# Optimization experiments

Hardware: AMD Instinct MI355X
Metric: run time of the kernel (lower is better)

## Reference

```python
import jax, jax.numpy as jnp
import numpy as np

NEG = -1e6  # SequenceMask fill value from original code


def setup_inputs() -> dict:
    key = jax.random.key(0)
    ks = jax.random.split(key, 7)
    B, Tq, Tk, U = 32, 1024, 1024, 256
    return {
        "query": jax.random.normal(ks[0], (B, Tq, U), dtype=jnp.float32),
        "key": jax.random.normal(ks[1], (B, Tk, U), dtype=jnp.float32),
        "value": jax.random.normal(ks[2], (B, Tk, U), dtype=jnp.float32),
        "valid_length": jax.random.randint(ks[3], (B,), 0, Tk, dtype=jnp.int32),
        "W_k": jax.random.normal(ks[4], (U, U), dtype=jnp.float32) * (1.0 / np.sqrt(U)),
        "W_q": jax.random.normal(ks[5], (U, U), dtype=jnp.float32) * (1.0 / np.sqrt(U)),
        "v": jax.random.normal(ks[6], (U,), dtype=jnp.float32) * (1.0 / np.sqrt(U)),
    }


def reference(query, key, value, valid_length, W_k, W_q, v):
    # Original applies W_k to query and W_q to key (naming swap kept faithfully).
    tq = jnp.tanh(jnp.einsum('bqu,vu->bqv', query, W_k))  # (B,Tq,U)
    tk = jnp.tanh(jnp.einsum('bku,vu->bkv', key, W_q))    # (B,Tk,U)
    # v is linear over (tq_i + tk_j): decompose to avoid (B,Tq,Tk,U) tensor.
    sq = jnp.einsum('bqu,u->bq', tq, v)  # (B,Tq)
    sk = jnp.einsum('bku,u->bk', tk, v)  # (B,Tk)
    scores = sq[:, :, None] + sk[:, None, :]  # (B,Tq,Tk)
    Tk_ = key.shape[1]
    mask = jnp.arange(Tk_)[None, None, :] < valid_length[:, None, None]  # (B,1,Tk)
    scores = jnp.where(mask, scores, NEG)
    attn = jax.nn.softmax(scores, axis=-1)  # dropout p=0 (eval) -> identity
    return jnp.einsum('bqk,bkd->bqd', attn, value)
```

## Files before the change

kernel.cpp:

```cpp
#include <hip/hip_runtime.h>
#include <hip/hip_fp16.h>
#include <math.h>

#define NB 32
#define TQ 1024
#define TK 1024
#define UD 256

typedef __attribute__((ext_vector_type(8))) _Float16 f16x8;
typedef __attribute__((ext_vector_type(4))) float f32x4;

__device__ __forceinline__ float fast_tanh(float x) {
  const float e = __expf(2.0f * x);
  return 1.0f - 2.0f / (e + 1.0f);
}

__global__ __launch_bounds__(256, 2) void sk_mfma_kernel(
    const float* __restrict__ key, const float* __restrict__ Wq,
    const float* __restrict__ v, float* __restrict__ sk) {
  __shared__ _Float16 Bt[32768];

  const int tid = threadIdx.x;
  const int lane = tid & 63;
  const int wc = tid >> 6;
  const int lx = lane & 15;
  const int lg = lane >> 4;
  const int arow = blockIdx.x * 64 + wc * 16 + lx;
  const float* gA = key + (size_t)arow * UD + lg * 8;

  f32x4 acc[16];
#pragma unroll
  for (int n = 0; n < 16; ++n) acc[n] = (f32x4){0.f, 0.f, 0.f, 0.f};

  for (int p = 0; p < 2; ++p) {
    {
      const float* wrow = Wq + (size_t)tid * UD + p * 128;
#pragma unroll
      for (int it = 0; it < 16; ++it) {
        const float4 w0 = *reinterpret_cast<const float4*>(wrow + it * 8);
        const float4 w1 = *reinterpret_cast<const float4*>(wrow + it * 8 + 4);
        f16x8 h;
        h[0] = (_Float16)w0.x; h[1] = (_Float16)w0.y;
        h[2] = (_Float16)w0.z; h[3] = (_Float16)w0.w;
        h[4] = (_Float16)w1.x; h[5] = (_Float16)w1.y;
        h[6] = (_Float16)w1.z; h[7] = (_Float16)w1.w;
        *reinterpret_cast<f16x8*>(Bt + ((size_t)it * 256 + tid) * 8) = h;
      }
    }
    __syncthreads();

#pragma unroll
    for (int kc = 0; kc < 4; ++kc) {
      const int k0 = p * 128 + kc * 32;
      const float4 a0 = *reinterpret_cast<const float4*>(gA + k0);
      const float4 a1 = *reinterpret_cast<const float4*>(gA + k0 + 4);
      f16x8 af;
      af[0] = (_Float16)a0.x; af[1] = (_Float16)a0.y;
      af[2] = (_Float16)a0.z; af[3] = (_Float16)a0.w;
      af[4] = (_Float16)a1.x; af[5] = (_Float16)a1.y;
      af[6] = (_Float16)a1.z; af[7] = (_Float16)a1.w;
#pragma unroll
      for (int n = 0; n < 16; ++n) {
        const f16x8 bf = *reinterpret_cast<const f16x8*>(
            Bt + (((kc * 4 + lg) * 256) + n * 16 + lx) * 8);
        acc[n] =
            __builtin_amdgcn_mfma_f32_16x16x32_f16(af, bf, acc[n], 0, 0, 0);
      }
    }
    __syncthreads();
  }

  float out_r[4] = {0.f, 0.f, 0.f, 0.f};
#pragma unroll
  for (int n = 0; n < 16; ++n) {
    const float vn = v[n * 16 + lx];
#pragma unroll
    for (int r = 0; r < 4; ++r) out_r[r] += vn * fast_tanh(acc[n][r]);
  }
#pragma unroll
  for (int r = 0; r < 4; ++r) {
    float s = out_r[r];
    s += __shfl_xor(s, 1);
    s += __shfl_xor(s, 2);
    s += __shfl_xor(s, 4);
    s += __shfl_xor(s, 8);
    if (lx == 0) sk[blockIdx.x * 64 + wc * 16 + lg * 4 + r] = s;
  }
}

__global__ __launch_bounds__(256) void pv_bcast_kernel(
    const float* __restrict__ sk, const int* __restrict__ vlen,
    const float* __restrict__ value, float* __restrict__ out) {
  const int b = blockIdx.x >> 3;
  const int dc = blockIdx.x & 7;
  const int tid = threadIdx.x;
  const int vl = vlen[b];
  __shared__ float wbuf[1024];
  __shared__ float red4[8];
  __shared__ float racc[32][32];
  __shared__ float fin[32];
  const float* skb = sk + b * TK;

  if (vl == 0) {
#pragma unroll
    for (int idx = 0; idx < 4; ++idx) wbuf[tid + idx * 256] = 1.0f / (float)TK;
  } else {
    float m = -1e30f;
#pragma unroll
    for (int idx = 0; idx < 4; ++idx) {
      const int k = tid + idx * 256;
      if (k < vl) m = fmaxf(m, skb[k]);
    }
    for (int off = 1; off < 64; off <<= 1) m = fmaxf(m, __shfl_xor(m, off));
    if ((tid & 63) == 0) red4[tid >> 6] = m;
    __syncthreads();
    m = fmaxf(fmaxf(red4[0], red4[1]), fmaxf(red4[2], red4[3]));
    float e[4];
    float zs = 0.f;
#pragma unroll
    for (int idx = 0; idx < 4; ++idx) {
      const int k = tid + idx * 256;
      e[idx] = (k < vl) ? __expf(skb[k] - m) : 0.f;
      zs += e[idx];
    }
    for (int off = 1; off < 64; off <<= 1) zs += __shfl_xor(zs, off);
    if ((tid & 63) == 0) red4[4 + (tid >> 6)] = zs;
    __syncthreads();
    const float rz = 1.0f / (red4[4] + red4[5] + red4[6] + red4[7]);
#pragma unroll
    for (int idx = 0; idx < 4; ++idx) wbuf[tid + idx * 256] = e[idx] * rz;
  }
  __syncthreads();

  const int c = tid & 7;
  const int kg = tid >> 3;
  const float* vb = value + (size_t)b * TK * UD + dc * 32 + c * 4;
  float4 a = make_float4(0.f, 0.f, 0.f, 0.f);
#pragma unroll 8
  for (int i = 0; i < 32; ++i) {
    const int k = i * 32 + kg;
    const float wk = wbuf[k];
    const float4 x = *reinterpret_cast<const float4*>(vb + (size_t)k * UD);
    a.x = fmaf(wk, x.x, a.x);
    a.y = fmaf(wk, x.y, a.y);
    a.z = fmaf(wk, x.z, a.z);
    a.w = fmaf(wk, x.w, a.w);
  }
  racc[kg][c * 4 + 0] = a.x;
  racc[kg][c * 4 + 1] = a.y;
  racc[kg][c * 4 + 2] = a.z;
  racc[kg][c * 4 + 3] = a.w;
  __syncthreads();
  if (tid < 32) {
    float s = 0.f;
#pragma unroll
    for (int g = 0; g < 32; ++g) s += racc[g][tid];
    fin[tid] = s;
  }
  __syncthreads();

  const float4 f4 = *reinterpret_cast<const float4*>(&fin[c * 4]);
  float* ob = out + (size_t)b * TQ * UD + dc * 32 + c * 4;
#pragma unroll 8
  for (int i = 0; i < 32; ++i) {
    const int q = i * 32 + kg;
    *reinterpret_cast<float4*>(ob + (size_t)q * UD) = f4;
  }
}

extern "C" void kernel_launch(void* const* d_in, const int* in_sizes, int n_in,
                              void* d_out, int out_size, void* d_ws,
                              size_t ws_size, hipStream_t stream) {
  const float* key = (const float*)d_in[1];
  const float* value = (const float*)d_in[2];
  const int* vlen = (const int*)d_in[3];
  const float* Wq = (const float*)d_in[5];
  const float* v = (const float*)d_in[6];
  float* out = (float*)d_out;

  float* sk = (float*)d_ws;

  sk_mfma_kernel<<<(NB * TK) / 64, 256, 0, stream>>>(key, Wq, v, sk);
  pv_bcast_kernel<<<NB * 8, 256, 0, stream>>>(sk, vlen, value, out);
}
```

Before: 43.79 us.

## Retile sk GEMM into 2x4 wave grid with staged A tiles, widen pv blocks

The sk kernel grows to 512 threads arranged as a 2x4 wave grid, each wave owning a 32x64 output tile. Both the key tile and a 64-wide K-slice of Wq go through shared memory in four phases, which shrinks LDS use and raises occupancy. A cross-wave reduction in LDS then forms the per-row v-weighted tanh sum. The pv_bcast kernel moves to 1024 threads with one score per thread and a two-level reduction, trading more barriers for more parallelism per batch block.

New measurement: 43.24 us. No clear change (-1.3%).

```diff
diff --git a/kernel.cpp b/kernel.cpp
--- a/kernel.cpp
+++ b/kernel.cpp
@@ -15,120 +15,154 @@
   return 1.0f - 2.0f / (e + 1.0f);
 }
 
-__global__ __launch_bounds__(256, 2) void sk_mfma_kernel(
+__device__ __forceinline__ f16x8 cvt2(const float4 a, const float4 b) {
+  f16x8 h;
+  h[0] = (_Float16)a.x; h[1] = (_Float16)a.y;
+  h[2] = (_Float16)a.z; h[3] = (_Float16)a.w;
+  h[4] = (_Float16)b.x; h[5] = (_Float16)b.y;
+  h[6] = (_Float16)b.z; h[7] = (_Float16)b.w;
+  return h;
+}
+
+__global__ __launch_bounds__(512, 4) void sk_mfma_kernel(
     const float* __restrict__ key, const float* __restrict__ Wq,
     const float* __restrict__ v, float* __restrict__ sk) {
-  __shared__ _Float16 Bt[32768];
+  __shared__ _Float16 Bt[8 * 256 * 8];
+  __shared__ _Float16 At[8 * 64 * 8];
 
   const int tid = threadIdx.x;
   const int lane = tid & 63;
-  const int wc = tid >> 6;
+  const int wid = tid >> 6;
+  const int wr = wid >> 2;
+  const int wc = wid & 3;
   const int lx = lane & 15;
   const int lg = lane >> 4;
-  const int arow = blockIdx.x * 64 + wc * 16 + lx;
-  const float* gA = key + (size_t)arow * UD + lg * 8;
-
-  f32x4 acc[16];
-#pragma unroll
-  for (int n = 0; n < 16; ++n) acc[n] = (f32x4){0.f, 0.f, 0.f, 0.f};
-
-  for (int p = 0; p < 2; ++p) {
+  const int row0 = blockIdx.x * 64;
+
+  const int ar = tid & 63, ah = tid >> 6;
+  const int bu = tid & 255, bg = tid >> 8;
+
+  f32x4 acc[2][4];
+#pragma unroll
+  for (int m = 0; m < 2; ++m)
+#pragma unroll
+    for (int n = 0; n < 4; ++n) acc[m][n] = (f32x4){0.f, 0.f, 0.f, 0.f};
+
+  for (int p = 0; p < 4; ++p) {
+    const int k0 = p * 64;
     {
-      const float* wrow = Wq + (size_t)tid * UD + p * 128;
-#pragma unroll
-      for (int it = 0; it < 16; ++it) {
-        const float4 w0 = *reinterpret_cast<const float4*>(wrow + it * 8);
-        const float4 w1 = *reinterpret_cast<const float4*>(wrow + it * 8 + 4);
-        f16x8 h;
-        h[0] = (_Float16)w0.x; h[1] = (_Float16)w0.y;
-        h[2] = (_Float16)w0.z; h[3] = (_Float16)w0.w;
-        h[4] = (_Float16)w1.x; h[5] = (_Float16)w1.y;
-        h[6] = (_Float16)w1.z; h[7] = (_Float16)w1.w;
-        *reinterpret_cast<f16x8*>(Bt + ((size_t)it * 256 + tid) * 8) = h;
+      const float* ga = key + (size_t)(row0 + ar) * UD + k0 + ah * 8;
+      const float4 a0 = *reinterpret_cast<const float4*>(ga);
+      const float4 a1 = *reinterpret_cast<const float4*>(ga + 4);
+      *reinterpret_cast<f16x8*>(At + ((ah << 6) + ar) * 8) = cvt2(a0, a1);
+    }
+    {
+      const float* gb = Wq + (size_t)bu * UD + k0 + bg * 32;
+#pragma unroll
+      for (int gg = 0; gg < 4; ++gg) {
+        const float4 b0 = *reinterpret_cast<const float4*>(gb + gg * 8);
+        const float4 b1 = *reinterpret_cast<const float4*>(gb + gg * 8 + 4);
+        const int ks = bg * 4 + gg;
+        *reinterpret_cast<f16x8*>(Bt + ((ks << 8) + bu) * 8) = cvt2(b0, b1);
       }
     }
     __syncthreads();
 
 #pragma unroll
-    for (int kc = 0; kc < 4; ++kc) {
-      const int k0 = p * 128 + kc * 32;
-      const float4 a0 = *reinterpret_cast<const float4*>(gA + k0);
-      const float4 a1 = *reinterpret_cast<const float4*>(gA + k0 + 4);
-      f16x8 af;
-      af[0] = (_Float16)a0.x; af[1] = (_Float16)a0.y;
-      af[2] = (_Float16)a0.z; af[3] = (_Float16)a0.w;
-      af[4] = (_Float16)a1.x; af[5] = (_Float16)a1.y;
-      af[6] = (_Float16)a1.z; af[7] = (_Float16)a1.w;
-#pragma unroll
-      for (int n = 0; n < 16; ++n) {
-        const f16x8 bf = *reinterpret_cast<const f16x8*>(
-            Bt + (((kc * 4 + lg) * 256) + n * 16 + lx) * 8);
-        acc[n] =
-            __builtin_amdgcn_mfma_f32_16x16x32_f16(af, bf, acc[n], 0, 0, 0);
-      }
-    }
-    __syncthreads();
-  }
-
-  float out_r[4] = {0.f, 0.f, 0.f, 0.f};
-#pragma unroll
-  for (int n = 0; n < 16; ++n) {
-    const float vn = v[n * 16 + lx];
-#pragma unroll
-    for (int r = 0; r < 4; ++r) out_r[r] += vn * fast_tanh(acc[n][r]);
-  }
-#pragma unroll
-  for (int r = 0; r < 4; ++r) {
-    float s = out_r[r];
-    s += __shfl_xor(s, 1);
-    s += __shfl_xor(s, 2);
-    s += __shfl_xor(s, 4);
-    s += __shfl_xor(s, 8);
-    if (lx == 0) sk[blockIdx.x * 64 + wc * 16 + lg * 4 + r] = s;
-  }
-}
-
-__global__ __launch_bounds__(256) void pv_bcast_kernel(
+    for (int kc = 0; kc < 2; ++kc) {
+      const int ks = kc * 4 + lg;
+      f16x8 af[2], bf[4];
+#pragma unroll
+      for (int m = 0; m < 2; ++m)
+        af[m] = *reinterpret_cast<const f16x8*>(
+            At + ((ks << 6) + wr * 32 + m * 16 + lx) * 8);
+#pragma unroll
+      for (int n = 0; n < 4; ++n)
+        bf[n] = *reinterpret_cast<const f16x8*>(
+            Bt + ((ks << 8) + wc * 64 + n * 16 + lx) * 8);
+#pragma unroll
+      for (int m = 0; m < 2; ++m)
+#pragma unroll
+        for (int n = 0; n < 4; ++n)
+          acc[m][n] = __builtin_amdgcn_mfma_f32_16x16x32_f16(af[m], bf[n],
+                                                             acc[m][n], 0, 0, 0);
+    }
+    __syncthreads();
+  }
+
+  float vv[4];
+#pragma unroll
+  for (int n = 0; n < 4; ++n) vv[n] = v[wc * 64 + n * 16 + lx];
+
+  float* red = (float*)At;
+  float part[2][4];
+#pragma unroll
+  for (int m = 0; m < 2; ++m)
+#pragma unroll
+    for (int r = 0; r < 4; ++r) part[m][r] = 0.f;
+#pragma unroll
+  for (int m = 0; m < 2; ++m)
+#pragma unroll
+    for (int n = 0; n < 4; ++n)
+#pragma unroll
+      for (int r = 0; r < 4; ++r)
+        part[m][r] += vv[n] * fast_tanh(acc[m][n][r]);
+
+#pragma unroll
+  for (int m = 0; m < 2; ++m)
+#pragma unroll
+    for (int r = 0; r < 4; ++r) {
+      float s = part[m][r];
+      s += __shfl_xor(s, 1);
+      s += __shfl_xor(s, 2);
+      s += __shfl_xor(s, 4);
+      s += __shfl_xor(s, 8);
+      if (lx == 0) red[(wr * 32 + m * 16 + lg * 4 + r) * 4 + wc] = s;
+    }
+  __syncthreads();
+  if (tid < 64) {
+    sk[row0 + tid] = red[tid * 4 + 0] + red[tid * 4 + 1] + red[tid * 4 + 2] +
+                     red[tid * 4 + 3];
+  }
+}
+
+__global__ __launch_bounds__(1024) void pv_bcast_kernel(
     const float* __restrict__ sk, const int* __restrict__ vlen,
     const float* __restrict__ value, float* __restrict__ out) {
   const int b = blockIdx.x >> 3;
   const int dc = blockIdx.x & 7;
   const int tid = threadIdx.x;
+  const int wid = tid >> 6;
   const int vl = vlen[b];
   __shared__ float wbuf[1024];
-  __shared__ float red4[8];
-  __shared__ float racc[32][32];
+  __shared__ float redm[16];
+  __shared__ float redz[16];
+  __shared__ float racc[128][36];
+  __shared__ float fin2[8][32];
   __shared__ float fin[32];
   const float* skb = sk + b * TK;
 
   if (vl == 0) {
-#pragma unroll
-    for (int idx = 0; idx < 4; ++idx) wbuf[tid + idx * 256] = 1.0f / (float)TK;
+    wbuf[tid] = 1.0f / (float)TK;
   } else {
-    float m = -1e30f;
-#pragma unroll
-    for (int idx = 0; idx < 4; ++idx) {
-      const int k = tid + idx * 256;
-      if (k < vl) m = fmaxf(m, skb[k]);
-    }
+    const float s = skb[tid];
+    const bool val = tid < vl;
+    float m = val ? s : -1e30f;
     for (int off = 1; off < 64; off <<= 1) m = fmaxf(m, __shfl_xor(m, off));
-    if ((tid & 63) == 0) red4[tid >> 6] = m;
-    __syncthreads();
-    m = fmaxf(fmaxf(red4[0], red4[1]), fmaxf(red4[2], red4[3]));
-    float e[4];
-    float zs = 0.f;
-#pragma unroll
-    for (int idx = 0; idx < 4; ++idx) {
-      const int k = tid + idx * 256;
-      e[idx] = (k < vl) ? __expf(skb[k] - m) : 0.f;
-      zs += e[idx];
-    }
+    if ((tid & 63) == 0) redm[wid] = m;
+    __syncthreads();
+    m = redm[0];
+#pragma unroll
+    for (int w = 1; w < 16; ++w) m = fmaxf(m, redm[w]);
+    const float e = val ? __expf(s - m) : 0.f;
+    float zs = e;
     for (int off = 1; off < 64; off <<= 1) zs += __shfl_xor(zs, off);
-    if ((tid & 63) == 0) red4[4 + (tid >> 6)] = zs;
-    __syncthreads();
-    const float rz = 1.0f / (red4[4] + red4[5] + red4[6] + red4[7]);
-#pragma unroll
-    for (int idx = 0; idx < 4; ++idx) wbuf[tid + idx * 256] = e[idx] * rz;
+    if ((tid & 63) == 0) redz[wid] = zs;
+    __syncthreads();
+    zs = redz[0];
+#pragma unroll
+    for (int w = 1; w < 16; ++w) zs += redz[w];
+    wbuf[tid] = e * (1.0f / zs);
   }
   __syncthreads();
 
@@ -136,9 +170,9 @@
   const int kg = tid >> 3;
   const float* vb = value + (size_t)b * TK * UD + dc * 32 + c * 4;
   float4 a = make_float4(0.f, 0.f, 0.f, 0.f);
-#pragma unroll 8
-  for (int i = 0; i < 32; ++i) {
-    const int k = i * 32 + kg;
+#pragma unroll
+  for (int i = 0; i < 8; ++i) {
+    const int k = i * 128 + kg;
     const float wk = wbuf[k];
     const float4 x = *reinterpret_cast<const float4*>(vb + (size_t)k * UD);
     a.x = fmaf(wk, x.x, a.x);
@@ -146,24 +180,31 @@
     a.z = fmaf(wk, x.z, a.z);
     a.w = fmaf(wk, x.w, a.w);
   }
-  racc[kg][c * 4 + 0] = a.x;
-  racc[kg][c * 4 + 1] = a.y;
-  racc[kg][c * 4 + 2] = a.z;
-  racc[kg][c * 4 + 3] = a.w;
+  *reinterpret_cast<float4*>(&racc[kg][c * 4]) = a;
+  __syncthreads();
+  if (tid < 256) {
+    const int d = tid & 31;
+    const int g = tid >> 5;
+    float s = 0.f;
+#pragma unroll
+    for (int j = 0; j < 16; ++j) s += racc[g * 16 + j][d];
+    fin2[g][d] = s;
+  }
   __syncthreads();
   if (tid < 32) {
     float s = 0.f;
 #pragma unroll
-    for (int g = 0; g < 32; ++g) s += racc[g][tid];
+    for (int g = 0; g < 8; ++g) s += fin2[g][tid];
     fin[tid] = s;
   }
   __syncthreads();
 
   const float4 f4 = *reinterpret_cast<const float4*>(&fin[c * 4]);
   float* ob = out + (size_t)b * TQ * UD + dc * 32 + c * 4;
-#pragma unroll 8
-  for (int i = 0; i < 32; ++i) {
-    const int q = i * 32 + kg;
+  const int qg = tid >> 3;
+#pragma unroll
+  for (int i = 0; i < 8; ++i) {
+    const int q = i * 128 + qg;
     *reinterpret_cast<float4*>(ob + (size_t)q * UD) = f4;
   }
 }
@@ -180,6 +221,6 @@
 
   float* sk = (float*)d_ws;
 
-  sk_mfma_kernel<<<(NB * TK) / 64, 256, 0, stream>>>(key, Wq, v, sk);
-  pv_bcast_kernel<<<NB * 8, 256, 0, stream>>>(sk, vlen, value, out);
-}
+  sk_mfma_kernel<<<(NB * TK) / 64, 512, 0, stream>>>(key, Wq, v, sk);
+  pv_bcast_kernel<<<NB * 8, 1024, 0, stream>>>(sk, vlen, value, out);
+}
```
